# Kernel optimization log

Measured on AMD Instinct MI355X. Metric: run time of the kernel, lower is better.

The kernel has to match this reference:

```python
import jax, jax.numpy as jnp
import numpy as np

E = 2048
H = 16
D = E // H  # head_dim = 128


def setup_inputs() -> dict:
    key = jax.random.key(0)
    ks = jax.random.split(key, 8)
    s = 0.02
    x = jax.random.normal(ks[0], (2, 2048, E), dtype=jnp.float32)
    Wq = jax.random.normal(ks[1], (E, E), dtype=jnp.float32) * s
    Wk = jax.random.normal(ks[2], (E, E), dtype=jnp.float32) * s
    Wv = jax.random.normal(ks[3], (E, E), dtype=jnp.float32) * s
    W1 = jax.random.normal(ks[4], (2 * E, E), dtype=jnp.float32) * s
    b1 = jax.random.normal(ks[5], (2 * E,), dtype=jnp.float32) * s
    W2 = jax.random.normal(ks[6], (E, 2 * E), dtype=jnp.float32) * s
    b2 = jax.random.normal(ks[7], (E,), dtype=jnp.float32) * s
    return {"x": x, "Wq": Wq, "Wk": Wk, "Wv": Wv, "W1": W1, "b1": b1, "W2": W2, "b2": b2}


def reference(x, Wq, Wk, Wv, W1, b1, W2, b2):
    B, S, _ = x.shape
    # QKV projections (torch Linear: x @ W.T), reshape to (B,S,H,D)
    q = (x @ Wq.T).reshape(B, S, H, D)
    k = (x @ Wk.T).reshape(B, S, H, D)
    v = (x @ Wv.T).reshape(B, S, H, D)
    # scores: (B,H,S,S)
    score = jnp.einsum('bqhd,bkhd->bhqk', q, k)
    # causal mask added BEFORE scaling (as in original; -inf unaffected by scale)
    causal = jnp.tril(jnp.ones((S, S), dtype=bool))
    score = jnp.where(causal, score, -jnp.inf)
    score = score / jnp.sqrt(jnp.float32(D))
    attn = jax.nn.softmax(score, axis=-1)
    o = jnp.einsum('bhqk,bkhd->bqhd', attn, v).reshape(B, S, E)
    # FFN with hidden = 2*E, no residual connections in this block
    h = jax.nn.gelu(o @ W1.T + b1)
    return h @ W2.T + b2
```

## Files before the change

### kernel.cpp

```cpp
#include <hip/hip_runtime.h>
#include <cmath>


typedef _Float16 half8 __attribute__((ext_vector_type(8)));
typedef _Float16 half4v __attribute__((ext_vector_type(4)));
typedef float float4v __attribute__((ext_vector_type(4)));

__device__ inline void load_lds16(const _Float16* g, _Float16* l) {
  __builtin_amdgcn_global_load_lds(
      (const __attribute__((address_space(1))) void*)g,
      (__attribute__((address_space(3))) void*)l, 16, 0, 0);
}

__global__ void cvt_kernel(const float* __restrict__ s0, const float* __restrict__ s1,
                           const float* __restrict__ s2, const float* __restrict__ s3,
                           _Float16* d0, _Float16* d1, _Float16* d2, _Float16* d3,
                           int n0, int n1, int n2, int n3, float sc1) {
  const float* s;
  _Float16* d;
  int n;
  float sc = 1.0f;
  switch (blockIdx.y) {
    case 0: s = s0; d = d0; n = n0; break;
    case 1: s = s1; d = d1; n = n1; sc = sc1; break;
    case 2: s = s2; d = d2; n = n2; break;
    default: s = s3; d = d3; n = n3; break;
  }
  const int step = gridDim.x * 256 * 4;
  for (int i = (blockIdx.x * 256 + threadIdx.x) * 4; i < n; i += step) {
    float4v v = *(const float4v*)&s[i];
    half4v h;
#pragma unroll
    for (int e = 0; e < 4; e++) h[e] = (_Float16)(v[e] * sc);
    *(half4v*)&d[i] = h;
  }
}

__device__ __forceinline__ void gemm8_core(
    const _Float16* __restrict__ A, const _Float16* __restrict__ B, int Kloop,
    int Kstride, int bm, int bn, _Float16* lds, float4v acc[8][4]) {
  const int tid = threadIdx.x;
  const int w = tid >> 6, lane = tid & 63;
  const int l16 = lane & 15, quad = lane >> 4;
  const int srow = w * 16 + (lane >> 2);
  const int clocal = ((lane & 3) * 8) ^ ((lane & 32) ? 16 : 0);
  int rdh = (l16 << 5) + (quad << 3);
  rdh ^= (l16 & 8) << 1;

  const _Float16* pA0 = A + (size_t)(bm + srow) * Kstride + clocal;
  const _Float16* pA1 = A + (size_t)(bm + 128 + srow) * Kstride + clocal;
  const _Float16* pB0 = B + (size_t)(bn + srow) * Kstride + clocal;
  const _Float16* pB1 = B + (size_t)(bn + 128 + srow) * Kstride + clocal;

  _Float16* const dA0 = lds + w * 1024;
  _Float16* const dA1 = lds + 8192 + w * 1024;
  _Float16* const dB0 = lds + 16384 + w * 1024;
  _Float16* const dB1 = lds + 24576 + w * 1024;

  const int aH = w >> 2, bH = (w >> 1) & 1, bRB = (w & 1) * 4;
  const _Float16* const rA0 = lds + aH * 8192;
  const _Float16* const rB0 = lds + 16384 + bH * 8192;
  const _Float16* const rA1 = rA0 + 32768;
  const _Float16* const rB1 = rB0 + 32768;

  const int NT = Kloop >> 6;

#define STG(p, d, kt)                     \
  do {                                    \
    const _Float16* _s = (p) + (kt) * 64; \
    load_lds16(_s, (d));                  \
    load_lds16(_s + 32, (d) + 512);       \
  } while (0)
#define BARRIER() asm volatile("s_barrier" ::: "memory")
#define WAIT_LGKM()                                  \
  asm volatile("s_waitcnt lgkmcnt(0)" ::: "memory"); \
  __builtin_amdgcn_sched_barrier(0);
#define RD_A(base, RB0)                                                       \
  _Pragma("unroll") for (int rb = 0; rb < 4; rb++)                            \
  _Pragma("unroll") for (int ks = 0; ks < 2; ks++)                            \
      af[rb][ks] = *(const half8*)&(base)[((((RB0) + rb) * 2 + ks) << 9) + rdh];
#define RD_B(base, J0)                                                        \
  _Pragma("unroll") for (int j = 0; j < 2; j++)                               \
  _Pragma("unroll") for (int ks = 0; ks < 2; ks++)                            \
      bf[(J0) + j][ks] =                                                      \
          *(const half8*)&(base)[(((bRB + (J0) + j) * 2 + ks) << 9) + rdh];
#define MFMA_Q(RB0, J0)                                                       \
  __builtin_amdgcn_s_setprio(1);                                              \
  _Pragma("unroll") for (int rb = 0; rb < 4; rb++)                            \
  _Pragma("unroll") for (int j = 0; j < 2; j++)                               \
  _Pragma("unroll") for (int ks = 0; ks < 2; ks++)                            \
      acc[(RB0) + rb][(J0) + j] = __builtin_amdgcn_mfma_f32_16x16x32_f16(     \
          af[rb][ks], bf[(J0) + j][ks], acc[(RB0) + rb][(J0) + j], 0, 0, 0);  \
  __builtin_amdgcn_s_setprio(0);                                              \
  BARRIER();

  STG(pB0, dB0, 0); STG(pB1, dB1, 0); STG(pA0, dA0, 0); STG(pA1, dA1, 0);
  STG(pB0, dB0 + 32768, 1); STG(pB1, dB1 + 32768, 1);
  asm volatile("s_waitcnt vmcnt(4)" ::: "memory");
  BARRIER();

  half8 af[4][2], bf[4][2];

  for (int t = 0; t < NT; t += 2) {
    const bool last = (t + 2 >= NT);
    RD_A(rA0, 0) RD_B(rB0, 0)
    STG(pA0, dA0 + 32768, t + 1);
    BARRIER(); WAIT_LGKM()
    MFMA_Q(0, 0)
    RD_B(rB0, 2)
    STG(pA1, dA1 + 32768, t + 1);
    BARRIER(); WAIT_LGKM()
    MFMA_Q(0, 2)
    RD_A(rA0, 4)
    if (!last) STG(pB0, dB0, t + 2);
    BARRIER(); WAIT_LGKM()
    MFMA_Q(4, 0)
    if (!last) {
      STG(pA0, dA0, t + 2);
      asm volatile("s_waitcnt vmcnt(4)" ::: "memory");
    } else {
      asm volatile("s_waitcnt vmcnt(0)" ::: "memory");
    }
    BARRIER();
    MFMA_Q(4, 2)
    RD_A(rA1, 0) RD_B(rB1, 0)
    if (!last) STG(pA1, dA1, t + 2);
    BARRIER(); WAIT_LGKM()
    MFMA_Q(0, 0)
    RD_B(rB1, 2)
    if (!last) STG(pB1, dB1, t + 2);
    BARRIER(); WAIT_LGKM()
    MFMA_Q(0, 2)
    RD_A(rA1, 4)
    if (!last) STG(pB0, dB0 + 32768, t + 3);
    BARRIER(); WAIT_LGKM()
    MFMA_Q(4, 0)
    if (!last) {
      STG(pB1, dB1 + 32768, t + 3);
      asm volatile("s_waitcnt vmcnt(4)" ::: "memory");
    }
    BARRIER();
    MFMA_Q(4, 2)
  }
#undef STG
#undef BARRIER
#undef WAIT_LGKM
#undef RD_A
#undef RD_B
#undef MFMA_Q
}

__global__ __launch_bounds__(512, 2) void gemm_qkv(
    const _Float16* __restrict__ xh, const _Float16* __restrict__ Wq,
    const _Float16* __restrict__ Wk, const _Float16* __restrict__ Wv,
    _Float16* __restrict__ Qh, _Float16* __restrict__ Kh,
    _Float16* __restrict__ Vt, const float* __restrict__ W1f,
    const float* __restrict__ W2f, _Float16* __restrict__ W1h,
    _Float16* __restrict__ W2h) {
  __shared__ __align__(16) _Float16 lds[67584];
  const int z = blockIdx.z;
  const int tid = threadIdx.x;
  if (z == 3) {
    const int bidx = blockIdx.x + (blockIdx.y << 3);
    const int step = 128 * 512 * 4;
    for (int i = (bidx * 512 + tid) * 4; i < 8388608; i += step) {
      float4v v1 = *(const float4v*)&W1f[i];
      float4v v2 = *(const float4v*)&W2f[i];
      half4v h1, h2;
#pragma unroll
      for (int e = 0; e < 4; e++) { h1[e] = (_Float16)v1[e]; h2[e] = (_Float16)v2[e]; }
      *(half4v*)&W1h[i] = h1;
      *(half4v*)&W2h[i] = h2;
    }
    return;
  }
  const _Float16* B = (z == 0) ? Wq : (z == 1 ? Wk : Wv);
  const int bm = blockIdx.y * 256, bn = blockIdx.x * 256;
  float4v acc[8][4] = {};
  gemm8_core(xh, B, 2048, 2048, bm, bn, lds, acc);

  const int w = tid >> 6, lane = tid & 63;
  const int l16 = lane & 15, quad = lane >> 4;
  const int wm = (w >> 2) * 128, wn = (w & 3) * 64;
  if (z == 2) {
    _Float16* Tr = lds;
    __syncthreads();
#pragma unroll
    for (int j = 0; j < 4; j++) {
      const int cl = wn + j * 16 + l16;
#pragma unroll
      for (int rb = 0; rb < 8; rb++) {
        const int ml = wm + rb * 16 + quad * 4;
#pragma unroll
        for (int reg = 0; reg < 4; reg++)
          Tr[cl * 264 + ml + reg] = (_Float16)acc[rb][j][reg];
      }
    }
    __syncthreads();
    const int cl = tid >> 1;
    const int ml = (tid & 1) * 128;
    const int mg = bm + ml;
    _Float16* dst = Vt + ((size_t)(mg >> 11) << 22) +
                    ((size_t)(bn + cl) << 11) + (mg & 2047);
#pragma unroll
    for (int i = 0; i < 16; i++)
      *(half8*)(dst + i * 8) = *(const half8*)&Tr[cl * 264 + ml + i * 8];
  } else {
    _Float16* outRM = z ? Kh : Qh;
#pragma unroll
    for (int j = 0; j < 4; j++) {
      const int col = bn + wn + j * 16 + l16;
#pragma unroll
      for (int rb = 0; rb < 8; rb++) {
        const int rbase = bm + wm + rb * 16 + quad * 4;
#pragma unroll
        for (int reg = 0; reg < 4; reg++)
          outRM[(size_t)(rbase + reg) * 2048 + col] = (_Float16)acc[rb][j][reg];
      }
    }
  }
}

__global__ __launch_bounds__(512, 2) void gemm_ffn1(
    const _Float16* __restrict__ A, const _Float16* __restrict__ B,
    const float* __restrict__ bias, _Float16* __restrict__ out, int N, int K) {
  __shared__ __align__(16) _Float16 lds[65536];
  const int bm = blockIdx.y * 256, bn = blockIdx.x * 256;
  float4v acc[8][4] = {};
  gemm8_core(A, B, K, K, bm, bn, lds, acc);

  const int tid = threadIdx.x;
  const int w = tid >> 6, lane = tid & 63;
  const int l16 = lane & 15, quad = lane >> 4;
  const int wm = (w >> 2) * 128, wn = (w & 3) * 64;
#pragma unroll
  for (int j = 0; j < 4; j++) {
    const int col = bn + wn + j * 16 + l16;
    const float bv = bias[col];
#pragma unroll
    for (int rb = 0; rb < 8; rb++) {
      const int rbase = bm + wm + rb * 16 + quad * 4;
#pragma unroll
      for (int reg = 0; reg < 4; reg++) {
        const int m = rbase + reg;
        const float x = acc[rb][j][reg] + bv;
        const float t = x + 0.044715f * x * x * x;
        const float e = exp2f(-2.302208198f * t);
        out[(size_t)m * N + col] = (_Float16)(x / (1.0f + e));
      }
    }
  }
}

__global__ __launch_bounds__(512, 2) void gemm_ffn2_atomic(
    const _Float16* __restrict__ A, const _Float16* __restrict__ B,
    const float* __restrict__ bias, float* __restrict__ out) {
  __shared__ __align__(16) _Float16 lds[65536];
  const int bm = blockIdx.y * 256, bn = blockIdx.x * 256;
  const int k0 = blockIdx.z * 2048;
  float4v acc[8][4] = {};
  gemm8_core(A + k0, B + k0, 2048, 4096, bm, bn, lds, acc);

  const int tid = threadIdx.x;
  const int w = tid >> 6, lane = tid & 63;
  const int l16 = lane & 15, quad = lane >> 4;
  const int wm = (w >> 2) * 128, wn = (w & 3) * 64;
#pragma unroll
  for (int j = 0; j < 4; j++) {
    const int col = bn + wn + j * 16 + l16;
    const float bv = blockIdx.z ? 0.0f : bias[col];
#pragma unroll
    for (int rb = 0; rb < 8; rb++) {
      const int rbase = bm + wm + rb * 16 + quad * 4;
#pragma unroll
      for (int reg = 0; reg < 4; reg++)
        atomicAdd(&out[(size_t)(rbase + reg) * 2048 + col],
                  acc[rb][j][reg] + bv);
    }
  }
}

__global__ __launch_bounds__(256, 2) void attn_mfma(
    const _Float16* __restrict__ Qh, const _Float16* __restrict__ Kh,
    const _Float16* __restrict__ Vt, _Float16* __restrict__ Oh) {
  __shared__ __align__(16) _Float16 Ksh[64][136];
  __shared__ __align__(16) _Float16 Vsh[128][72];
  __shared__ __align__(16) _Float16 Psh[4][32][72];

  const int b = blockIdx.z;
  int qt = blockIdx.x;
  if (b) qt = gridDim.x - 1 - qt;
  const int h = blockIdx.y;
  const int tid = threadIdx.x;
  const int wave = tid >> 6, lane = tid & 63;
  const int l16 = lane & 15, quad = lane >> 4;
  const int q0 = qt * 128;
  const int wq0 = q0 + wave * 32;

  half8 qf[2][4];
#pragma unroll
  for (int rb = 0; rb < 2; rb++)
#pragma unroll
    for (int kc = 0; kc < 4; kc++)
      qf[rb][kc] = *(const half8*)(Qh +
          (size_t)(b * 2048 + wq0 + rb * 16 + l16) * 2048 + h * 128 +
          kc * 32 + quad * 8);

  half8 ones;
#pragma unroll
  for (int e = 0; e < 8; e++) ones[e] = (_Float16)1.0f;

  const int kkey = tid >> 2, kd = (tid & 3) * 32;
  const int vd = tid >> 1, vkey = (tid & 1) * 32;

  half8 kpre[4], vpre[4];
  {
    const _Float16* p = Kh + (size_t)(b * 2048 + kkey) * 2048 + h * 128 + kd;
#pragma unroll
    for (int i = 0; i < 4; i++) kpre[i] = *(const half8*)(p + i * 8);
    const _Float16* pv = Vt + ((size_t)b << 22) + (size_t)(h * 128 + vd) * 2048 + vkey;
#pragma unroll
    for (int i = 0; i < 4; i++) vpre[i] = *(const half8*)(pv + i * 8);
  }

  float4v o[2][9] = {};
  float4v mrow[2];
#pragma unroll
  for (int rb = 0; rb < 2; rb++)
#pragma unroll
    for (int e = 0; e < 4; e++) mrow[rb][e] = -INFINITY;

  const int nkb = qt * 2 + 2;
  for (int kb = 0; kb < nkb; kb++) {
    const int k0 = kb * 64;
    __syncthreads();
#pragma unroll
    for (int i = 0; i < 4; i++) *(half8*)&Ksh[kkey][kd + i * 8] = kpre[i];
#pragma unroll
    for (int i = 0; i < 4; i++) *(half8*)&Vsh[vd][vkey + i * 8] = vpre[i];
    __syncthreads();

    if (kb + 1 < nkb) {
      const int k1 = k0 + 64;
      const _Float16* p = Kh + (size_t)(b * 2048 + k1 + kkey) * 2048 + h * 128 + kd;
#pragma unroll
      for (int i = 0; i < 4; i++) kpre[i] = *(const half8*)(p + i * 8);
      const _Float16* pv = Vt + ((size_t)b << 22) + (size_t)(h * 128 + vd) * 2048 + k1 + vkey;
#pragma unroll
      for (int i = 0; i < 4; i++) vpre[i] = *(const half8*)(pv + i * 8);
    }

    if (k0 <= wq0 + 31) {
      float4v s[2][4] = {};
#pragma unroll
      for (int kc = 0; kc < 4; kc++) {
#pragma unroll
        for (int cb = 0; cb < 4; cb++) {
          half8 kf = *(const half8*)&Ksh[cb * 16 + l16][kc * 32 + quad * 8];
#pragma unroll
          for (int rb = 0; rb < 2; rb++)
            s[rb][cb] = __builtin_amdgcn_mfma_f32_16x16x32_f16(qf[rb][kc], kf, s[rb][cb], 0, 0, 0);
        }
      }
      if (k0 + 63 > wq0) {
#pragma unroll
        for (int cb = 0; cb < 4; cb++)
#pragma unroll
          for (int rb = 0; rb < 2; rb++)
#pragma unroll
            for (int reg = 0; reg < 4; reg++) {
              const int key = k0 + cb * 16 + l16;
              const int row = wq0 + rb * 16 + quad * 4 + reg;
              if (key > row) s[rb][cb][reg] = -INFINITY;
            }
      }
#pragma unroll
      for (int rb = 0; rb < 2; rb++) {
        float4v mt;
#pragma unroll
        for (int e = 0; e < 4; e++)
          mt[e] = fmaxf(fmaxf(s[rb][0][e], s[rb][1][e]),
                        fmaxf(s[rb][2][e], s[rb][3][e]));
        int need = 0;
#pragma unroll
        for (int e = 0; e < 4; e++) need |= (mt[e] > mrow[rb][e] + 8.0f) ? 1 : 0;
        if (__any(need)) {
#pragma unroll
          for (int msk = 1; msk <= 8; msk <<= 1)
#pragma unroll
            for (int e = 0; e < 4; e++) mt[e] = fmaxf(mt[e], __shfl_xor(mt[e], msk, 64));
          float4v al;
#pragma unroll
          for (int e = 0; e < 4; e++) {
            const float mn = fmaxf(mrow[rb][e], mt[e]);
            al[e] = exp2f(mrow[rb][e] - mn);
            mrow[rb][e] = mn;
          }
#pragma unroll
          for (int cd = 0; cd < 9; cd++)
#pragma unroll
            for (int e = 0; e < 4; e++) o[rb][cd][e] *= al[e];
        }
#pragma unroll
        for (int cb = 0; cb < 4; cb++) {
#pragma unroll
          for (int e = 0; e < 4; e++) s[rb][cb][e] = exp2f(s[rb][cb][e] - mrow[rb][e]);
#pragma unroll
          for (int e = 0; e < 4; e++)
            Psh[wave][rb * 16 + quad * 4 + e][cb * 16 + l16] = (_Float16)s[rb][cb][e];
        }
      }
      half8 pf[2][2];
#pragma unroll
      for (int rb = 0; rb < 2; rb++)
#pragma unroll
        for (int kc = 0; kc < 2; kc++)
          pf[rb][kc] = *(const half8*)&Psh[wave][rb * 16 + l16][kc * 32 + quad * 8];
#pragma unroll
      for (int cd = 0; cd < 8; cd++) {
#pragma unroll
        for (int kc = 0; kc < 2; kc++) {
          half8 vf = *(const half8*)&Vsh[cd * 16 + l16][kc * 32 + quad * 8];
#pragma unroll
          for (int rb = 0; rb < 2; rb++)
            o[rb][cd] = __builtin_amdgcn_mfma_f32_16x16x32_f16(pf[rb][kc], vf, o[rb][cd], 0, 0, 0);
        }
      }
#pragma unroll
      for (int kc = 0; kc < 2; kc++)
#pragma unroll
        for (int rb = 0; rb < 2; rb++)
          o[rb][8] = __builtin_amdgcn_mfma_f32_16x16x32_f16(pf[rb][kc], ones, o[rb][8], 0, 0, 0);
    }
  }

#pragma unroll
  for (int rb = 0; rb < 2; rb++) {
    float4v inv;
#pragma unroll
    for (int e = 0; e < 4; e++) inv[e] = 1.0f / o[rb][8][e];
#pragma unroll
    for (int cd = 0; cd < 8; cd++)
#pragma unroll
      for (int reg = 0; reg < 4; reg++)
        Oh[(size_t)(b * 2048 + wq0 + rb * 16 + quad * 4 + reg) * 2048 +
           h * 128 + cd * 16 + l16] = (_Float16)(o[rb][cd][reg] * inv[reg]);
  }
}

extern "C" void kernel_launch(void* const* d_in, const int* in_sizes, int n_in,
                              void* d_out, int out_size, void* d_ws,
                              size_t ws_size, hipStream_t stream) {
  const float* x = (const float*)d_in[0];
  const float* Wq = (const float*)d_in[1];
  const float* Wk = (const float*)d_in[2];
  const float* Wv = (const float*)d_in[3];
  const float* W1 = (const float*)d_in[4];
  const float* b1 = (const float*)d_in[5];
  const float* W2 = (const float*)d_in[6];
  const float* b2 = (const float*)d_in[7];
  float* out = (float*)d_out;

  const int ME = 8388608;
  const int EE = 4194304;

  _Float16* ws = (_Float16*)d_ws;
  _Float16* xh  = ws;
  _Float16* Wqh = xh + ME;
  _Float16* Wkh = Wqh + EE;
  _Float16* Wvh = Wkh + EE;
  _Float16* Qh  = Wvh + EE;
  _Float16* Kh  = Qh + ME;
  _Float16* Vt  = Kh + ME;
  _Float16* Oh  = xh;
  _Float16* Hid = Qh;

  const size_t need = ((size_t)ME * 4 + (size_t)EE * 3 + (size_t)ME * 2) * 2;
  const bool fused = ws_size >= need;
  _Float16* W1h = fused ? (Vt + ME) : Wqh;
  _Float16* W2h = fused ? (Vt + ME + ME) : Vt;

  const float qscale = 1.4426950408889634f * 0.08838834764831845f;

  cvt_kernel<<<dim3(1024, 4), 256, 0, stream>>>(x, Wq, Wk, Wv, xh, Wqh, Wkh, Wvh,
                                                ME, EE, EE, EE, qscale);
  gemm_qkv<<<dim3(8, 16, fused ? 4 : 3), 512, 0, stream>>>(
      xh, Wqh, Wkh, Wvh, Qh, Kh, Vt, W1, W2, W1h, W2h);
  attn_mfma<<<dim3(16, 16, 2), 256, 0, stream>>>(Qh, Kh, Vt, Oh);
  if (!fused)
    cvt_kernel<<<dim3(1024, 2), 256, 0, stream>>>(W1, W2, nullptr, nullptr,
                                                  W1h, W2h, nullptr, nullptr,
                                                  ME, ME, 0, 0, 1.0f);
  gemm_ffn1<<<dim3(16, 16), 512, 0, stream>>>(Oh, W1h, b1, Hid, 4096, 2048);
  gemm_ffn2_atomic<<<dim3(8, 16, 2), 512, 0, stream>>>(Hid, W2h, b2, out);
}
```

Measured before the change: 529.6 us.

## Batch GEMM global-to-LDS prefetches and widen fp16 conversion loops to 8 elements

Regroups the global-to-LDS staging in the GEMM main loop so all A and B tiles for a buffer are issued together, with vmcnt waits raised from 4 to 8. More loads are in flight per wait, but the prefetches are now clustered at fewer points rather than spread across the MFMA phases. Separately, the fp32-to-fp16 conversion loops (input converter and the W1/W2 path in the QKV kernel) now handle 8 elements per thread with 16-byte half8 stores. This halves the loop iterations and widens the stores.

```diff
diff --git a/kernel.cpp b/kernel.cpp
--- a/kernel.cpp
+++ b/kernel.cpp
@@ -26,13 +26,17 @@
     case 2: s = s2; d = d2; n = n2; break;
     default: s = s3; d = d3; n = n3; break;
   }
-  const int step = gridDim.x * 256 * 4;
-  for (int i = (blockIdx.x * 256 + threadIdx.x) * 4; i < n; i += step) {
-    float4v v = *(const float4v*)&s[i];
-    half4v h;
-#pragma unroll
-    for (int e = 0; e < 4; e++) h[e] = (_Float16)(v[e] * sc);
-    *(half4v*)&d[i] = h;
+  const int step = gridDim.x * 256 * 8;
+  for (int i = (blockIdx.x * 256 + threadIdx.x) * 8; i < n; i += step) {
+    float4v v0 = *(const float4v*)&s[i];
+    float4v v1 = *(const float4v*)&s[i + 4];
+    half8 h;
+#pragma unroll
+    for (int e = 0; e < 4; e++) {
+      h[e] = (_Float16)(v0[e] * sc);
+      h[e + 4] = (_Float16)(v1[e] * sc);
+    }
+    *(half8*)&d[i] = h;
   }
 }
 
@@ -96,7 +100,8 @@
 
   STG(pB0, dB0, 0); STG(pB1, dB1, 0); STG(pA0, dA0, 0); STG(pA1, dA1, 0);
   STG(pB0, dB0 + 32768, 1); STG(pB1, dB1 + 32768, 1);
-  asm volatile("s_waitcnt vmcnt(4)" ::: "memory");
+  STG(pA0, dA0 + 32768, 1); STG(pA1, dA1 + 32768, 1);
+  asm volatile("s_waitcnt vmcnt(8)" ::: "memory");
   BARRIER();
 
   half8 af[4][2], bf[4][2];
@@ -104,40 +109,36 @@
   for (int t = 0; t < NT; t += 2) {
     const bool last = (t + 2 >= NT);
     RD_A(rA0, 0) RD_B(rB0, 0)
-    STG(pA0, dA0 + 32768, t + 1);
     BARRIER(); WAIT_LGKM()
     MFMA_Q(0, 0)
     RD_B(rB0, 2)
-    STG(pA1, dA1 + 32768, t + 1);
     BARRIER(); WAIT_LGKM()
     MFMA_Q(0, 2)
     RD_A(rA0, 4)
-    if (!last) STG(pB0, dB0, t + 2);
+    if (!last) { STG(pB0, dB0, t + 2); STG(pB1, dB1, t + 2); }
     BARRIER(); WAIT_LGKM()
     MFMA_Q(4, 0)
     if (!last) {
-      STG(pA0, dA0, t + 2);
-      asm volatile("s_waitcnt vmcnt(4)" ::: "memory");
+      STG(pA0, dA0, t + 2); STG(pA1, dA1, t + 2);
+      asm volatile("s_waitcnt vmcnt(8)" ::: "memory");
     } else {
       asm volatile("s_waitcnt vmcnt(0)" ::: "memory");
     }
     BARRIER();
     MFMA_Q(4, 2)
     RD_A(rA1, 0) RD_B(rB1, 0)
-    if (!last) STG(pA1, dA1, t + 2);
     BARRIER(); WAIT_LGKM()
     MFMA_Q(0, 0)
     RD_B(rB1, 2)
-    if (!last) STG(pB1, dB1, t + 2);
     BARRIER(); WAIT_LGKM()
     MFMA_Q(0, 2)
     RD_A(rA1, 4)
-    if (!last) STG(pB0, dB0 + 32768, t + 3);
+    if (!last) { STG(pB0, dB0 + 32768, t + 3); STG(pB1, dB1 + 32768, t + 3); }
     BARRIER(); WAIT_LGKM()
     MFMA_Q(4, 0)
     if (!last) {
-      STG(pB1, dB1 + 32768, t + 3);
-      asm volatile("s_waitcnt vmcnt(4)" ::: "memory");
+      STG(pA0, dA0 + 32768, t + 3); STG(pA1, dA1 + 32768, t + 3);
+      asm volatile("s_waitcnt vmcnt(8)" ::: "memory");
     }
     BARRIER();
     MFMA_Q(4, 2)
@@ -162,15 +163,20 @@
   const int tid = threadIdx.x;
   if (z == 3) {
     const int bidx = blockIdx.x + (blockIdx.y << 3);
-    const int step = 128 * 512 * 4;
-    for (int i = (bidx * 512 + tid) * 4; i < 8388608; i += step) {
-      float4v v1 = *(const float4v*)&W1f[i];
-      float4v v2 = *(const float4v*)&W2f[i];
-      half4v h1, h2;
-#pragma unroll
-      for (int e = 0; e < 4; e++) { h1[e] = (_Float16)v1[e]; h2[e] = (_Float16)v2[e]; }
-      *(half4v*)&W1h[i] = h1;
-      *(half4v*)&W2h[i] = h2;
+    const int step = 128 * 512 * 8;
+    for (int i = (bidx * 512 + tid) * 8; i < 8388608; i += step) {
+      float4v a0 = *(const float4v*)&W1f[i];
+      float4v a1 = *(const float4v*)&W1f[i + 4];
+      float4v b0 = *(const float4v*)&W2f[i];
+      float4v b1 = *(const float4v*)&W2f[i + 4];
+      half8 h1, h2;
+#pragma unroll
+      for (int e = 0; e < 4; e++) {
+        h1[e] = (_Float16)a0[e]; h1[e + 4] = (_Float16)a1[e];
+        h2[e] = (_Float16)b0[e]; h2[e + 4] = (_Float16)b1[e];
+      }
+      *(half8*)&W1h[i] = h1;
+      *(half8*)&W2h[i] = h2;
     }
     return;
   }
```

Result: slower. 543.6 us (+2.6%).
